# Kernel optimization log

Measured on AMD Instinct MI355X. Metric: run time of the kernel, lower is better.

Reference implementation:

```python
import jax, jax.numpy as jnp
import numpy as np

NEG_SLOPE = 0.2

def gat_layer(x, src, dst, W, a_src, a_dst, b):
    # PyG GATConv (concat=True, self-loops already appended to src/dst)
    N = x.shape[0]
    H, C = a_src.shape
    h = (x @ W).reshape(N, H, C)                      # [N,H,C]
    alpha_s = jnp.einsum('nhc,hc->nh', h, a_src)      # [N,H]
    alpha_d = jnp.einsum('nhc,hc->nh', h, a_dst)
    e = jax.nn.leaky_relu(alpha_s[src] + alpha_d[dst], NEG_SLOPE)  # [E,H]
    # scatter-softmax over edges grouped by destination node
    m = jax.ops.segment_max(e, dst, num_segments=N)
    e = jnp.exp(e - m[dst])
    denom = jax.ops.segment_sum(e, dst, num_segments=N)
    alpha = e / (denom[dst] + 1e-16)                  # [E,H]
    msg = h[src] * alpha[:, :, None]                  # [E,H,C]
    out = jax.ops.segment_sum(msg, dst, num_segments=N)
    return out.reshape(N, H * C) + b


def setup_inputs() -> dict:
    key = jax.random.key(0)
    ks = jax.random.split(key, 16)
    N, E, B = 20000, 640000, 32
    in_f, out_dim = 128, 512
    x = jax.random.normal(ks[0], (N, in_f), dtype=jnp.float32)
    edge_index = jax.random.randint(ks[1], (2, E), 0, N, dtype=jnp.int64)
    batch = jnp.sort(jax.random.randint(ks[2], (N,), 0, B, dtype=jnp.int64))
    def p(k, shape):
        return jax.random.normal(k, shape, dtype=jnp.float32) * 0.1
    inp = {
        'x': x, 'edge_index': edge_index, 'batch': batch,
        'W1': p(ks[3], (in_f, 256)), 'a1_src': p(ks[4], (4, 64)), 'a1_dst': p(ks[5], (4, 64)), 'b1': jnp.zeros((256,), jnp.float32),
        'W2': p(ks[6], (256, 256)), 'a2_src': p(ks[7], (4, 64)), 'a2_dst': p(ks[8], (4, 64)), 'b2': jnp.zeros((256,), jnp.float32),
        'W3': p(ks[9], (256, 256)), 'a3_src': p(ks[10], (4, 64)), 'a3_dst': p(ks[11], (4, 64)), 'b3': jnp.zeros((256,), jnp.float32),
        'W4': p(ks[12], (256, 512)), 'a4_src': p(ks[13], (4, 128)), 'a4_dst': p(ks[14], (4, 128)), 'b4': jnp.zeros((512,), jnp.float32),
        'fcW': p(ks[15], (1024, out_dim)), 'fcb': jnp.zeros((out_dim,), jnp.float32),
    }
    return inp


def reference(x, edge_index, batch, W1, a1_src, a1_dst, b1, W2, a2_src, a2_dst, b2,
              W3, a3_src, a3_dst, b3, W4, a4_src, a4_dst, b4, fcW, fcb):
    N = x.shape[0]
    B = 32
    loops = jnp.arange(N, dtype=edge_index.dtype)
    src = jnp.concatenate([edge_index[0], loops])
    dst = jnp.concatenate([edge_index[1], loops])
    h = jax.nn.elu(gat_layer(x, src, dst, W1, a1_src, a1_dst, b1))
    h = jax.nn.elu(gat_layer(h, src, dst, W2, a2_src, a2_dst, b2))
    h = jax.nn.elu(gat_layer(h, src, dst, W3, a3_src, a3_dst, b3))
    h = jax.nn.elu(gat_layer(h, src, dst, W4, a4_src, a4_dst, b4))   # [N,512]
    cnt = jax.ops.segment_sum(jnp.ones((N,), h.dtype), batch, num_segments=B)
    x_mean = jax.ops.segment_sum(h, batch, num_segments=B) / jnp.maximum(cnt, 1.0)[:, None]
    x_max = jax.ops.segment_max(h, batch, num_segments=B)
    x_max = jnp.where(jnp.isfinite(x_max), x_max, 0.0)
    g = jnp.concatenate([x_mean, x_max], axis=1)                     # [B,1024]
    return g @ fcW + fcb
```

## Files before the change

kernel.cpp:

```cpp
#include <hip/hip_runtime.h>
#include <math.h>

#define WAVE 64

typedef __attribute__((ext_vector_type(4))) float f32x4;
typedef _Float16 h16x4 __attribute__((ext_vector_type(4)));
typedef _Float16 h16x8 __attribute__((ext_vector_type(8)));

__device__ __forceinline__ float selh(float e0, float e1, float e2, float e3, int m){
  float r = (m == 1) ? e1 : e0;
  r = (m == 2) ? e2 : r;
  r = (m == 3) ? e3 : r;
  return r;
}

__global__ void k_zero_i(int* p, int n){
  int i = blockIdx.x*blockDim.x + threadIdx.x;
  if (i < n) p[i] = 0;
}

__global__ void k_zero_f(float* p, int n){
  int i = blockIdx.x*blockDim.x + threadIdx.x;
  if (i < n) p[i] = 0.f;
}

__global__ void k_count(const int* __restrict__ ei, int E, int N, int* __restrict__ cnt){
  int i = blockIdx.x*blockDim.x + threadIdx.x;
  if (i >= E + N) return;
  int d = (i < E) ? ei[E + i] : (i - E);
  atomicAdd(&cnt[d], 1);
}

__global__ __launch_bounds__(1024)
void k_scan1(const int* __restrict__ cnt, int* __restrict__ rp, int* __restrict__ bsum, int N){
  __shared__ int sd[1024];
  int t = threadIdx.x, i = blockIdx.x*1024 + t;
  int v = (i < N) ? cnt[i] : 0;
  sd[t] = v;
  __syncthreads();
  for (int off = 1; off < 1024; off <<= 1){
    int x = (t >= off) ? sd[t-off] : 0;
    __syncthreads();
    sd[t] += x;
    __syncthreads();
  }
  if (i < N) rp[i] = sd[t] - v;
  if (t == 1023) bsum[blockIdx.x] = sd[1023];
}

__global__ void k_scan2(int* __restrict__ bsum, int nb, int* __restrict__ rp, int N){
  int t = threadIdx.x;
  int orig = (t < nb) ? bsum[t] : 0;
  int v = orig;
  #pragma unroll
  for (int off = 1; off < 64; off <<= 1){
    int x = __shfl_up(v, off, WAVE);
    if (t >= off) v += x;
  }
  if (t < nb) bsum[t] = v - orig;
  if (t == 63) rp[N] = v;
}

__global__ __launch_bounds__(1024)
void k_scan3(int* __restrict__ rp, const int* __restrict__ bsum, int N){
  int i = blockIdx.x*1024 + threadIdx.x;
  if (i < N) rp[i] += bsum[blockIdx.x];
}

__global__ void k_copy_i(const int* __restrict__ a, int* __restrict__ b, int n){
  int i = blockIdx.x*blockDim.x + threadIdx.x;
  if (i < n) b[i] = a[i];
}

__global__ void k_fill(const int* __restrict__ ei, int E, int N,
                       int* __restrict__ cur, int* __restrict__ es){
  int i = blockIdx.x*blockDim.x + threadIdx.x;
  if (i >= E + N) return;
  int s, d;
  if (i < E){ s = ei[i]; d = ei[E + i]; } else { s = d = i - E; }
  int pos = atomicAdd(&cur[d], 1);
  es[pos] = s;
}

__global__ void k_bounds(const int* __restrict__ batch, int N, int B, int* __restrict__ bs){
  int b = blockIdx.x*blockDim.x + threadIdx.x;
  if (b > B) return;
  int lo = 0, hi = N;
  while (lo < hi){ int mid = (lo + hi) >> 1; if (batch[mid] < b) lo = mid + 1; else hi = mid; }
  bs[b] = lo;
}

__global__ __launch_bounds__(256)
void k_cvt16(const float* __restrict__ in, _Float16* __restrict__ out, int n4){
  int i = blockIdx.x*blockDim.x + threadIdx.x;
  if (i >= n4) return;
  float4 v = ((const float4*)in)[i];
  h16x4 o;
  o[0] = (_Float16)v.x; o[1] = (_Float16)v.y;
  o[2] = (_Float16)v.z; o[3] = (_Float16)v.w;
  ((h16x4*)out)[i] = o;
}

__global__ __launch_bounds__(256)
void k_cvt_w16(const float* __restrict__ W, _Float16* __restrict__ wt, int K, int Nc){
  int i = blockIdx.x*blockDim.x + threadIdx.x;
  if (i >= K*Nc) return;
  int k = i / Nc, n = i - k*Nc;
  wt[(size_t)n*K + k] = (_Float16)W[i];
}

template<int CHEAD>
__global__ __launch_bounds__(512)
void k_gemm_fused(const _Float16* __restrict__ Ax, const _Float16* __restrict__ Bw,
                  _Float16* __restrict__ Ch,
                  const float* __restrict__ asr, const float* __restrict__ adt,
                  float* __restrict__ as4, float* __restrict__ ad4,
                  int M, int K, int Nc){
  constexpr int LDP = 40;
  __shared__ _Float16 sA[128*LDP], sB[128*LDP];
  const int tid = threadIdx.x;
  const int m0 = blockIdx.x*128, n0 = blockIdx.y*128;
  const int w = tid >> 6, l = tid & 63;
  const int wr = w >> 1, wc = w & 1;
  const int sr = tid >> 2, sc = (tid & 3)*8;

  f32x4 acc00={0.f,0.f,0.f,0.f}, acc01=acc00, acc02=acc00, acc03=acc00;
  f32x4 acc10=acc00, acc11=acc00, acc12=acc00, acc13=acc00;

  const int arow = m0 + sr;
  const bool aval = arow < M;
  const size_t aoff = (size_t)arow*K + sc;
  const size_t boff = (size_t)(n0 + sr)*K + sc;

  const int fa0 = (wr*32 + (l & 15))*LDP + (l >> 4)*8;
  const int fa1 = fa0 + 16*LDP;
  const int fb0 = (wc*64 + (l & 15))*LDP + (l >> 4)*8;

  for (int k0 = 0; k0 < K; k0 += 32){
    uint4 va = make_uint4(0,0,0,0);
    if (aval) va = *(const uint4*)(Ax + aoff + k0);
    uint4 vb = *(const uint4*)(Bw + boff + k0);
    __syncthreads();
    *(uint4*)&sA[sr*LDP + sc] = va;
    *(uint4*)&sB[sr*LDP + sc] = vb;
    __syncthreads();

    h16x8 a0 = *(const h16x8*)&sA[fa0];
    h16x8 a1 = *(const h16x8*)&sA[fa1];

    h16x8 b;
    b = *(const h16x8*)&sB[fb0];
    acc00 = __builtin_amdgcn_mfma_f32_16x16x32_f16(a0, b, acc00, 0, 0, 0);
    acc10 = __builtin_amdgcn_mfma_f32_16x16x32_f16(a1, b, acc10, 0, 0, 0);
    b = *(const h16x8*)&sB[fb0 + 16*LDP];
    acc01 = __builtin_amdgcn_mfma_f32_16x16x32_f16(a0, b, acc01, 0, 0, 0);
    acc11 = __builtin_amdgcn_mfma_f32_16x16x32_f16(a1, b, acc11, 0, 0, 0);
    b = *(const h16x8*)&sB[fb0 + 32*LDP];
    acc02 = __builtin_amdgcn_mfma_f32_16x16x32_f16(a0, b, acc02, 0, 0, 0);
    acc12 = __builtin_amdgcn_mfma_f32_16x16x32_f16(a1, b, acc12, 0, 0, 0);
    b = *(const h16x8*)&sB[fb0 + 48*LDP];
    acc03 = __builtin_amdgcn_mfma_f32_16x16x32_f16(a0, b, acc03, 0, 0, 0);
    acc13 = __builtin_amdgcn_mfma_f32_16x16x32_f16(a1, b, acc13, 0, 0, 0);
  }

  const int colb = n0 + wc*64 + (l & 15);
  const int hy = (n0 + wc*64) / CHEAD;
  const float ca0 = asr[colb], ca1 = asr[colb+16], ca2 = asr[colb+32], ca3 = asr[colb+48];
  const float cd0 = adt[colb], cd1 = adt[colb+16], cd2 = adt[colb+32], cd3 = adt[colb+48];

  {
    const int rb = m0 + wr*32 + (l >> 4)*4;
    #pragma unroll
    for (int j = 0; j < 4; ++j){
      int row = rb + j;
      if (row < M){
        _Float16* hp = Ch + (size_t)row*Nc + colb;
        hp[0]  = (_Float16)acc00[j];
        hp[16] = (_Float16)acc01[j];
        hp[32] = (_Float16)acc02[j];
        hp[48] = (_Float16)acc03[j];
      }
      float ps = ca0*acc00[j] + ca1*acc01[j] + ca2*acc02[j] + ca3*acc03[j];
      float pd = cd0*acc00[j] + cd1*acc01[j] + cd2*acc02[j] + cd3*acc03[j];
      ps += __shfl_xor(ps, 1, WAVE);  pd += __shfl_xor(pd, 1, WAVE);
      ps += __shfl_xor(ps, 2, WAVE);  pd += __shfl_xor(pd, 2, WAVE);
      ps += __shfl_xor(ps, 4, WAVE);  pd += __shfl_xor(pd, 4, WAVE);
      ps += __shfl_xor(ps, 8, WAVE);  pd += __shfl_xor(pd, 8, WAVE);
      if ((l & 15) == 0 && row < M){
        atomicAdd(&as4[(size_t)row*4 + hy], ps);
        atomicAdd(&ad4[(size_t)row*4 + hy], pd);
      }
    }
  }
  {
    const int rb = m0 + wr*32 + 16 + (l >> 4)*4;
    #pragma unroll
    for (int j = 0; j < 4; ++j){
      int row = rb + j;
      if (row < M){
        _Float16* hp = Ch + (size_t)row*Nc + colb;
        hp[0]  = (_Float16)acc10[j];
        hp[16] = (_Float16)acc11[j];
        hp[32] = (_Float16)acc12[j];
        hp[48] = (_Float16)acc13[j];
      }
      float ps = ca0*acc10[j] + ca1*acc11[j] + ca2*acc12[j] + ca3*acc13[j];
      float pd = cd0*acc10[j] + cd1*acc11[j] + cd2*acc12[j] + cd3*acc13[j];
      ps += __shfl_xor(ps, 1, WAVE);  pd += __shfl_xor(pd, 1, WAVE);
      ps += __shfl_xor(ps, 2, WAVE);  pd += __shfl_xor(pd, 2, WAVE);
      ps += __shfl_xor(ps, 4, WAVE);  pd += __shfl_xor(pd, 4, WAVE);
      ps += __shfl_xor(ps, 8, WAVE);  pd += __shfl_xor(pd, 8, WAVE);
      if ((l & 15) == 0 && row < M){
        atomicAdd(&as4[(size_t)row*4 + hy], ps);
        atomicAdd(&ad4[(size_t)row*4 + hy], pd);
      }
    }
  }
}

template<int HC, int WF32>
__global__ __launch_bounds__(256)
void k_agg_h(const int* __restrict__ rp, const int* __restrict__ es,
             const float* __restrict__ as4, const float* __restrict__ ad4,
             const _Float16* __restrict__ h, const float* __restrict__ bias,
             float* __restrict__ outF, _Float16* __restrict__ oH, int N){
  constexpr int VEC = HC / 64;
  int wid  = (blockIdx.x*blockDim.x + threadIdx.x) >> 6;
  int lane = threadIdx.x & 63;
  if (wid >= N) return;
  int beg = rp[wid], end = rp[wid+1];

  const float4 adv = *(const float4*)(ad4 + (size_t)wid*4);
  const float ad0 = adv.x, ad1 = adv.y, ad2 = adv.z, ad3 = adv.w;

  float m0=-1e30f, m1=-1e30f, m2=-1e30f, m3=-1e30f;
  float s0=0.f, s1=0.f, s2=0.f, s3=0.f;
  for (int i = beg + lane; i < end; i += WAVE){
    int s = es[i];
    const float4 av = *(const float4*)(as4 + (size_t)s*4);
    float e, mn;
    e = av.x + ad0; e = (e >= 0.f) ? e : 0.2f*e;
    mn = fmaxf(m0, e); s0 = s0*__expf(m0-mn) + __expf(e-mn); m0 = mn;
    e = av.y + ad1; e = (e >= 0.f) ? e : 0.2f*e;
    mn = fmaxf(m1, e); s1 = s1*__expf(m1-mn) + __expf(e-mn); m1 = mn;
    e = av.z + ad2; e = (e >= 0.f) ? e : 0.2f*e;
    mn = fmaxf(m2, e); s2 = s2*__expf(m2-mn) + __expf(e-mn); m2 = mn;
    e = av.w + ad3; e = (e >= 0.f) ? e : 0.2f*e;
    mn = fmaxf(m3, e); s3 = s3*__expf(m3-mn) + __expf(e-mn); m3 = mn;
  }
  #pragma unroll
  for (int off = 32; off > 0; off >>= 1){
    float mo, so, mn;
    mo = __shfl_xor(m0, off, WAVE); so = __shfl_xor(s0, off, WAVE);
    mn = fmaxf(m0, mo); s0 = s0*__expf(m0-mn) + so*__expf(mo-mn); m0 = mn;
    mo = __shfl_xor(m1, off, WAVE); so = __shfl_xor(s1, off, WAVE);
    mn = fmaxf(m1, mo); s1 = s1*__expf(m1-mn) + so*__expf(mo-mn); m1 = mn;
    mo = __shfl_xor(m2, off, WAVE); so = __shfl_xor(s2, off, WAVE);
    mn = fmaxf(m2, mo); s2 = s2*__expf(m2-mn) + so*__expf(mo-mn); m2 = mn;
    mo = __shfl_xor(m3, off, WAVE); so = __shfl_xor(s3, off, WAVE);
    mn = fmaxf(m3, mo); s3 = s3*__expf(m3-mn) + so*__expf(mo-mn); m3 = mn;
  }
  const float i0 = 1.f/(s0 + 1e-16f), i1 = 1.f/(s1 + 1e-16f);
  const float i2 = 1.f/(s2 + 1e-16f), i3 = 1.f/(s3 + 1e-16f);
  const int myh = lane >> 4;

  float ac[VEC] = {};

  for (int cb = beg; cb < end; cb += WAVE){
    int nn = min(WAVE, end - cb);
    int sidx = 0;
    float w0 = 0.f, w1 = 0.f, w2 = 0.f, w3 = 0.f;
    if (cb + lane < end){
      sidx = es[cb + lane];
      const float4 av = *(const float4*)(as4 + (size_t)sidx*4);
      float e;
      e = av.x + ad0; e = (e >= 0.f) ? e : 0.2f*e; w0 = __expf(e - m0)*i0;
      e = av.y + ad1; e = (e >= 0.f) ? e : 0.2f*e; w1 = __expf(e - m1)*i1;
      e = av.z + ad2; e = (e >= 0.f) ? e : 0.2f*e; w2 = __expf(e - m2)*i2;
      e = av.w + ad3; e = (e >= 0.f) ? e : 0.2f*e; w3 = __expf(e - m3)*i3;
    }

    int j = 0;
    for (; j + 4 <= nn; j += 4){
      int sj0 = __shfl(sidx, j+0, WAVE), sj1 = __shfl(sidx, j+1, WAVE);
      int sj2 = __shfl(sidx, j+2, WAVE), sj3 = __shfl(sidx, j+3, WAVE);
      float u0 = selh(__shfl(w0,j+0,WAVE), __shfl(w1,j+0,WAVE), __shfl(w2,j+0,WAVE), __shfl(w3,j+0,WAVE), myh);
      float u1 = selh(__shfl(w0,j+1,WAVE), __shfl(w1,j+1,WAVE), __shfl(w2,j+1,WAVE), __shfl(w3,j+1,WAVE), myh);
      float u2 = selh(__shfl(w0,j+2,WAVE), __shfl(w1,j+2,WAVE), __shfl(w2,j+2,WAVE), __shfl(w3,j+2,WAVE), myh);
      float u3 = selh(__shfl(w0,j+3,WAVE), __shfl(w1,j+3,WAVE), __shfl(w2,j+3,WAVE), __shfl(w3,j+3,WAVE), myh);
      if (VEC == 4){
        h16x4 v0 = *(const h16x4*)(h + (size_t)sj0*HC + lane*4);
        h16x4 v1 = *(const h16x4*)(h + (size_t)sj1*HC + lane*4);
        h16x4 v2 = *(const h16x4*)(h + (size_t)sj2*HC + lane*4);
        h16x4 v3 = *(const h16x4*)(h + (size_t)sj3*HC + lane*4);
        #pragma unroll
        for (int c = 0; c < 4; ++c)
          ac[c] = fmaf(u0,(float)v0[c], fmaf(u1,(float)v1[c], fmaf(u2,(float)v2[c], fmaf(u3,(float)v3[c], ac[c]))));
      } else {
        h16x8 v0 = *(const h16x8*)(h + (size_t)sj0*HC + lane*8);
        h16x8 v1 = *(const h16x8*)(h + (size_t)sj1*HC + lane*8);
        h16x8 v2 = *(const h16x8*)(h + (size_t)sj2*HC + lane*8);
        h16x8 v3 = *(const h16x8*)(h + (size_t)sj3*HC + lane*8);
        #pragma unroll
        for (int c = 0; c < VEC; ++c)
          ac[c] = fmaf(u0,(float)v0[c], fmaf(u1,(float)v1[c], fmaf(u2,(float)v2[c], fmaf(u3,(float)v3[c], ac[c]))));
      }
    }
    for (; j < nn; ++j){
      int sj = __shfl(sidx, j, WAVE);
      float u = selh(__shfl(w0,j,WAVE), __shfl(w1,j,WAVE), __shfl(w2,j,WAVE), __shfl(w3,j,WAVE), myh);
      if (VEC == 4){
        h16x4 v = *(const h16x4*)(h + (size_t)sj*HC + lane*4);
        #pragma unroll
        for (int c = 0; c < 4; ++c) ac[c] = fmaf(u, (float)v[c], ac[c]);
      } else {
        h16x8 v = *(const h16x8*)(h + (size_t)sj*HC + lane*8);
        #pragma unroll
        for (int c = 0; c < VEC; ++c) ac[c] = fmaf(u, (float)v[c], ac[c]);
      }
    }
  }

  float r0=0,r1=0,r2=0,r3=0,r4=0,r5=0,r6=0,r7=0;
  {
    const float* bp = bias + lane*VEC;
    #pragma unroll
    for (int c = 0; c < VEC; ++c){
      float r = ac[c] + bp[c];
      r = r > 0.f ? r : expm1f(r);
      if (c==0) r0=r; else if (c==1) r1=r; else if (c==2) r2=r; else if (c==3) r3=r;
      else if (c==4) r4=r; else if (c==5) r5=r; else if (c==6) r6=r; else r7=r;
    }
  }
  if (WF32){
    float* op = outF + (size_t)wid*HC + lane*VEC;
    *(float4*)op = make_float4(r0,r1,r2,r3);
    if (VEC == 8) *(float4*)(op+4) = make_float4(r4,r5,r6,r7);
  } else {
    h16x4 o;
    o[0] = (_Float16)r0; o[1] = (_Float16)r1;
    o[2] = (_Float16)r2; o[3] = (_Float16)r3;
    *(h16x4*)(oH + (size_t)wid*HC + lane*VEC) = o;
    if (VEC == 8){
      h16x4 o2;
      o2[0] = (_Float16)r4; o2[1] = (_Float16)r5;
      o2[2] = (_Float16)r6; o2[3] = (_Float16)r7;
      *(h16x4*)(oH + (size_t)wid*HC + lane*VEC + 4) = o2;
    }
  }
}

__global__ void k_pool_partial(const float* __restrict__ h, const int* __restrict__ bs,
                               float* __restrict__ psum, float* __restrict__ pmax){
  int b = blockIdx.x, ch = blockIdx.y;
  int f = threadIdx.x;
  int s = bs[b], e = bs[b+1];
  long long len = e - s;
  int i0 = s + (int)(len * ch / 8);
  int i1 = s + (int)(len * (ch+1) / 8);
  float sm = 0.f, mx = -3.0e38f;
  for (int i = i0; i < i1; ++i){
    float v = h[(size_t)i*512 + f];
    sm += v; mx = fmaxf(mx, v);
  }
  int idx = (b*8 + ch)*512 + f;
  psum[idx] = sm; pmax[idx] = mx;
}

__global__ void k_pool_final(const float* __restrict__ psum, const float* __restrict__ pmax,
                             const int* __restrict__ bs, float* __restrict__ g){
  int b = blockIdx.x, f = threadIdx.x;
  float sm = 0.f, mx = -3.0e38f;
  for (int c = 0; c < 8; ++c){
    int idx = (b*8 + c)*512 + f;
    sm += psum[idx]; mx = fmaxf(mx, pmax[idx]);
  }
  int cnt = bs[b+1] - bs[b];
  g[b*1024 + f] = sm / fmaxf((float)cnt, 1.f);
  g[b*1024 + 512 + f] = (mx > -1e37f) ? mx : 0.f;
}

__global__ __launch_bounds__(256)
void k_fc(const float* __restrict__ g, const float* __restrict__ fcW,
          const float* __restrict__ fcb, float* __restrict__ out){
  __shared__ float gs[1024];
  __shared__ float red[4][64];
  int b = blockIdx.x, t = threadIdx.x;
  int o0 = blockIdx.y * 64;
  for (int i = t; i < 1024; i += 256) gs[i] = g[b*1024 + i];
  __syncthreads();
  int ol = t & 63, q = t >> 6;
  const float* wp = fcW + (size_t)(q*256)*512 + o0 + ol;
  float acc = 0.f;
  #pragma unroll 8
  for (int k = 0; k < 256; ++k)
    acc = fmaf(gs[q*256 + k], wp[(size_t)k*512], acc);
  red[q][ol] = acc;
  __syncthreads();
  if (t < 64){
    float r = red[0][t] + red[1][t] + red[2][t] + red[3][t] + fcb[o0 + t];
    out[b*512 + o0 + t] = r;
  }
}

extern "C" void kernel_launch(void* const* d_in, const int* in_sizes, int n_in,
                              void* d_out, int out_size, void* d_ws, size_t ws_size,
                              hipStream_t stream){
  (void)n_in; (void)out_size; (void)ws_size;
  const float* x     = (const float*)d_in[0];
  const int*   ei    = (const int*)d_in[1];
  const int*   batch = (const int*)d_in[2];
  const float* W[4]   = {(const float*)d_in[3],(const float*)d_in[7],(const float*)d_in[11],(const float*)d_in[15]};
  const float* asr[4] = {(const float*)d_in[4],(const float*)d_in[8],(const float*)d_in[12],(const float*)d_in[16]};
  const float* adt[4] = {(const float*)d_in[5],(const float*)d_in[9],(const float*)d_in[13],(const float*)d_in[17]};
  const float* bb[4]  = {(const float*)d_in[6],(const float*)d_in[10],(const float*)d_in[14],(const float*)d_in[18]};
  const float* fcW = (const float*)d_in[19];
  const float* fcb = (const float*)d_in[20];

  const int N  = in_sizes[0] / 128;
  const int E  = in_sizes[1] / 2;
  const int EN = E + N;
  const int B  = 32;
  const int NB = (N + 1023) / 1024;

  char* p = (char*)d_ws;
  auto alloc = [&](size_t bytes){ void* r = (void*)p; p += (bytes + 255) & ~(size_t)255; return r; };
  float* bufA = (float*)alloc((size_t)N*512*4);
  _Float16* hA = (_Float16*)alloc((size_t)N*512*2);
  _Float16* hB = (_Float16*)alloc((size_t)N*512*2);
  _Float16* Wh = (_Float16*)alloc((size_t)512*256*2);
  float* a2   = (float*)alloc((size_t)N*8*4);
  float* as4 = a2;
  float* ad4 = a2 + (size_t)N*4;
  int*   cnt  = (int*)alloc((size_t)N*4);
  int*   rp   = (int*)alloc((size_t)(N+1)*4);
  int*   cur  = (int*)alloc((size_t)N*4);
  int*   es   = (int*)alloc((size_t)EN*4);
  int*   bs   = (int*)alloc((size_t)(B+1)*4);
  int*   bsum = (int*)alloc((size_t)64*4);
  float* gpo  = (float*)alloc((size_t)B*1024*4);
  float* psum = (float*)alloc((size_t)B*8*512*4);
  float* pmax = (float*)alloc((size_t)B*8*512*4);

  k_zero_i<<<(N+255)/256, 256, 0, stream>>>(cnt, N);
  k_count<<<(EN+255)/256, 256, 0, stream>>>(ei, E, N, cnt);
  k_scan1<<<NB, 1024, 0, stream>>>(cnt, rp, bsum, N);
  k_scan2<<<1, 64, 0, stream>>>(bsum, NB, rp, N);
  k_scan3<<<NB, 1024, 0, stream>>>(rp, bsum, N);
  k_copy_i<<<(N+255)/256, 256, 0, stream>>>(rp, cur, N);
  k_fill<<<(EN+255)/256, 256, 0, stream>>>(ei, E, N, cur, es);
  k_bounds<<<1, 64, 0, stream>>>(batch, N, B, bs);

  const int wgrid = (N + 3) / 4;

  k_cvt16<<<((N*128/4) + 255)/256, 256, 0, stream>>>(x, hB, N*128/4);

  const int Kd[4]  = {128, 256, 256, 256};
  const int HCd[4] = {256, 256, 256, 512};

  for (int L = 0; L < 4; ++L){
    const int K = Kd[L], Nc = HCd[L];
    k_zero_f<<<(N*8 + 255)/256, 256, 0, stream>>>(a2, N*8);
    k_cvt_w16<<<(K*Nc + 255)/256, 256, 0, stream>>>(W[L], Wh, K, Nc);
    dim3 gg((N + 127)/128, Nc/128);
    if (Nc == 256)
      k_gemm_fused<64><<<gg, 512, 0, stream>>>(hB, Wh, hA, asr[L], adt[L], as4, ad4, N, K, Nc);
    else
      k_gemm_fused<128><<<gg, 512, 0, stream>>>(hB, Wh, hA, asr[L], adt[L], as4, ad4, N, K, Nc);
    if (L < 3)
      k_agg_h<256,0><<<wgrid, 256, 0, stream>>>(rp, es, as4, ad4, hA, bb[L], (float*)nullptr, hB, N);
    else
      k_agg_h<512,1><<<wgrid, 256, 0, stream>>>(rp, es, as4, ad4, hA, bb[L], bufA, (_Float16*)nullptr, N);
  }

  dim3 pg(B, 8);
  k_pool_partial<<<pg, 512, 0, stream>>>(bufA, bs, psum, pmax);
  k_pool_final<<<B, 512, 0, stream>>>(psum, pmax, bs, gpo);
  dim3 fg(B, 8);
  k_fc<<<fg, 256, 0, stream>>>(gpo, fcW, fcb, (float*)d_out);
}
```

Baseline: 490.8 us.

## Double-buffer GEMM LDS, drop attention-logit atomics, batch weight conversion and fuse copies

The GEMM main loop now double-buffers the shared-memory tiles, prefetching the next K slice while MFMAs run, so only one barrier is needed per step. Per-row attention logits are written directly, or reduced through shared memory for the 128-wide heads, instead of accumulated with atomics. This removes the per-layer zeroing kernel. All four weight matrices are converted in a single launch, and the cur copy is folded into the scan fixup kernel, cutting the launch count. The cost is twice the LDS use per block and an extra barrier in the epilogue for the wide-head layer.

After: 447.8 us. 8.8% less time.

```diff
diff --git a/kernel.cpp b/kernel.cpp
--- a/kernel.cpp
+++ b/kernel.cpp
@@ -17,11 +17,6 @@
 __global__ void k_zero_i(int* p, int n){
   int i = blockIdx.x*blockDim.x + threadIdx.x;
   if (i < n) p[i] = 0;
-}
-
-__global__ void k_zero_f(float* p, int n){
-  int i = blockIdx.x*blockDim.x + threadIdx.x;
-  if (i < n) p[i] = 0.f;
 }
 
 __global__ void k_count(const int* __restrict__ ei, int E, int N, int* __restrict__ cnt){
@@ -62,14 +57,13 @@
 }
 
 __global__ __launch_bounds__(1024)
-void k_scan3(int* __restrict__ rp, const int* __restrict__ bsum, int N){
+void k_scan3(int* __restrict__ rp, int* __restrict__ cur, const int* __restrict__ bsum, int N){
   int i = blockIdx.x*1024 + threadIdx.x;
-  if (i < N) rp[i] += bsum[blockIdx.x];
-}
-
-__global__ void k_copy_i(const int* __restrict__ a, int* __restrict__ b, int n){
-  int i = blockIdx.x*blockDim.x + threadIdx.x;
-  if (i < n) b[i] = a[i];
+  if (i < N){
+    int v = rp[i] + bsum[blockIdx.x];
+    rp[i] = v;
+    cur[i] = v;
+  }
 }
 
 __global__ void k_fill(const int* __restrict__ ei, int E, int N,
@@ -102,11 +96,26 @@
 }
 
 __global__ __launch_bounds__(256)
-void k_cvt_w16(const float* __restrict__ W, _Float16* __restrict__ wt, int K, int Nc){
+void k_cvt_w_all(const float* __restrict__ W0, const float* __restrict__ W1,
+                 const float* __restrict__ W2, const float* __restrict__ W3,
+                 _Float16* __restrict__ out){
   int i = blockIdx.x*blockDim.x + threadIdx.x;
-  if (i >= K*Nc) return;
-  int k = i / Nc, n = i - k*Nc;
-  wt[(size_t)n*K + k] = (_Float16)W[i];
+  if (i < 32768){
+    int k = i >> 8, n = i & 255;
+    out[(size_t)n*128 + k] = (_Float16)W0[i];
+  } else if (i < 98304){
+    int j = i - 32768;
+    int k = j >> 8, n = j & 255;
+    out[32768 + (size_t)n*256 + k] = (_Float16)W1[j];
+  } else if (i < 163840){
+    int j = i - 98304;
+    int k = j >> 8, n = j & 255;
+    out[98304 + (size_t)n*256 + k] = (_Float16)W2[j];
+  } else if (i < 294912){
+    int j = i - 163840;
+    int k = j >> 9, n = j & 511;
+    out[163840 + (size_t)n*256 + k] = (_Float16)W3[j];
+  }
 }
 
 template<int CHEAD>
@@ -117,7 +126,7 @@
                   float* __restrict__ as4, float* __restrict__ ad4,
                   int M, int K, int Nc){
   constexpr int LDP = 40;
-  __shared__ _Float16 sA[128*LDP], sB[128*LDP];
+  __shared__ _Float16 sA[2][128*LDP], sB[2][128*LDP];
   const int tid = threadIdx.x;
   const int m0 = blockIdx.x*128, n0 = blockIdx.y*128;
   const int w = tid >> 6, l = tid & 63;
@@ -135,39 +144,55 @@
   const int fa0 = (wr*32 + (l & 15))*LDP + (l >> 4)*8;
   const int fa1 = fa0 + 16*LDP;
   const int fb0 = (wc*64 + (l & 15))*LDP + (l >> 4)*8;
-
-  for (int k0 = 0; k0 < K; k0 += 32){
-    uint4 va = make_uint4(0,0,0,0);
-    if (aval) va = *(const uint4*)(Ax + aoff + k0);
-    uint4 vb = *(const uint4*)(Bw + boff + k0);
-    __syncthreads();
-    *(uint4*)&sA[sr*LDP + sc] = va;
-    *(uint4*)&sB[sr*LDP + sc] = vb;
-    __syncthreads();
-
-    h16x8 a0 = *(const h16x8*)&sA[fa0];
-    h16x8 a1 = *(const h16x8*)&sA[fa1];
-
+  const int steps = K >> 5;
+
+  uint4 va = make_uint4(0,0,0,0), vb;
+  if (aval) va = *(const uint4*)(Ax + aoff);
+  vb = *(const uint4*)(Bw + boff);
+  *(uint4*)&sA[0][sr*LDP + sc] = va;
+  *(uint4*)&sB[0][sr*LDP + sc] = vb;
+  __syncthreads();
+
+  for (int ks = 0; ks < steps; ++ks){
+    const int cur = ks & 1;
+    const bool more = (ks + 1 < steps);
+    if (more){
+      const int k0 = (ks + 1)*32;
+      va = make_uint4(0,0,0,0);
+      if (aval) va = *(const uint4*)(Ax + aoff + k0);
+      vb = *(const uint4*)(Bw + boff + k0);
+    }
+
+    h16x8 a0 = *(const h16x8*)&sA[cur][fa0];
+    h16x8 a1 = *(const h16x8*)&sA[cur][fa1];
     h16x8 b;
-    b = *(const h16x8*)&sB[fb0];
+    b = *(const h16x8*)&sB[cur][fb0];
     acc00 = __builtin_amdgcn_mfma_f32_16x16x32_f16(a0, b, acc00, 0, 0, 0);
     acc10 = __builtin_amdgcn_mfma_f32_16x16x32_f16(a1, b, acc10, 0, 0, 0);
-    b = *(const h16x8*)&sB[fb0 + 16*LDP];
+    b = *(const h16x8*)&sB[cur][fb0 + 16*LDP];
     acc01 = __builtin_amdgcn_mfma_f32_16x16x32_f16(a0, b, acc01, 0, 0, 0);
     acc11 = __builtin_amdgcn_mfma_f32_16x16x32_f16(a1, b, acc11, 0, 0, 0);
-    b = *(const h16x8*)&sB[fb0 + 32*LDP];
+    b = *(const h16x8*)&sB[cur][fb0 + 32*LDP];
     acc02 = __builtin_amdgcn_mfma_f32_16x16x32_f16(a0, b, acc02, 0, 0, 0);
     acc12 = __builtin_amdgcn_mfma_f32_16x16x32_f16(a1, b, acc12, 0, 0, 0);
-    b = *(const h16x8*)&sB[fb0 + 48*LDP];
+    b = *(const h16x8*)&sB[cur][fb0 + 48*LDP];
     acc03 = __builtin_amdgcn_mfma_f32_16x16x32_f16(a0, b, acc03, 0, 0, 0);
     acc13 = __builtin_amdgcn_mfma_f32_16x16x32_f16(a1, b, acc13, 0, 0, 0);
+
+    if (more){
+      *(uint4*)&sA[cur^1][sr*LDP + sc] = va;
+      *(uint4*)&sB[cur^1][sr*LDP + sc] = vb;
+      __syncthreads();
+    }
   }
 
   const int colb = n0 + wc*64 + (l & 15);
-  const int hy = (n0 + wc*64) / CHEAD;
   const float ca0 = asr[colb], ca1 = asr[colb+16], ca2 = asr[colb+32], ca3 = asr[colb+48];
   const float cd0 = adt[colb], cd1 = adt[colb+16], cd2 = adt[colb+32], cd3 = adt[colb+48];
 
+  float psA[1]; (void)psA;
+
+  float psm0[4], pdm0[4], psm1[4], pdm1[4];
   {
     const int rb = m0 + wr*32 + (l >> 4)*4;
     #pragma unroll
@@ -186,10 +211,7 @@
       ps += __shfl_xor(ps, 2, WAVE);  pd += __shfl_xor(pd, 2, WAVE);
       ps += __shfl_xor(ps, 4, WAVE);  pd += __shfl_xor(pd, 4, WAVE);
       ps += __shfl_xor(ps, 8, WAVE);  pd += __shfl_xor(pd, 8, WAVE);
-      if ((l & 15) == 0 && row < M){
-        atomicAdd(&as4[(size_t)row*4 + hy], ps);
-        atomicAdd(&ad4[(size_t)row*4 + hy], pd);
-      }
+      psm0[j] = ps; pdm0[j] = pd;
     }
   }
   {
@@ -210,9 +232,51 @@
       ps += __shfl_xor(ps, 2, WAVE);  pd += __shfl_xor(pd, 2, WAVE);
       ps += __shfl_xor(ps, 4, WAVE);  pd += __shfl_xor(pd, 4, WAVE);
       ps += __shfl_xor(ps, 8, WAVE);  pd += __shfl_xor(pd, 8, WAVE);
-      if ((l & 15) == 0 && row < M){
-        atomicAdd(&as4[(size_t)row*4 + hy], ps);
-        atomicAdd(&ad4[(size_t)row*4 + hy], pd);
+      psm1[j] = ps; pdm1[j] = pd;
+    }
+  }
+
+  if (CHEAD == 64){
+    const int hy = blockIdx.y*2 + wc;
+    if ((l & 15) == 0){
+      const int rb0 = m0 + wr*32 + (l >> 4)*4;
+      #pragma unroll
+      for (int j = 0; j < 4; ++j){
+        int row = rb0 + j;
+        if (row < M){ as4[(size_t)row*4 + hy] = psm0[j]; ad4[(size_t)row*4 + hy] = pdm0[j]; }
+      }
+      const int rb1 = rb0 + 16;
+      #pragma unroll
+      for (int j = 0; j < 4; ++j){
+        int row = rb1 + j;
+        if (row < M){ as4[(size_t)row*4 + hy] = psm1[j]; ad4[(size_t)row*4 + hy] = pdm1[j]; }
+      }
+    }
+  } else {
+    float* red = (float*)&sA[0][0];
+    __syncthreads();
+    if ((l & 15) == 0){
+      const int lr0 = wr*32 + (l >> 4)*4;
+      #pragma unroll
+      for (int j = 0; j < 4; ++j){
+        red[(lr0 + j)*4 + wc*2 + 0] = psm0[j];
+        red[(lr0 + j)*4 + wc*2 + 1] = pdm0[j];
+      }
+      const int lr1 = lr0 + 16;
+      #pragma unroll
+      for (int j = 0; j < 4; ++j){
+        red[(lr1 + j)*4 + wc*2 + 0] = psm1[j];
+        red[(lr1 + j)*4 + wc*2 + 1] = pdm1[j];
+      }
+    }
+    __syncthreads();
+    if (tid < 128){
+      int row = m0 + tid;
+      if (row < M){
+        float ps = red[tid*4 + 0] + red[tid*4 + 2];
+        float pd = red[tid*4 + 1] + red[tid*4 + 3];
+        as4[(size_t)row*4 + blockIdx.y] = ps;
+        ad4[(size_t)row*4 + blockIdx.y] = pd;
       }
     }
   }
@@ -428,7 +492,7 @@
   float* bufA = (float*)alloc((size_t)N*512*4);
   _Float16* hA = (_Float16*)alloc((size_t)N*512*2);
   _Float16* hB = (_Float16*)alloc((size_t)N*512*2);
-  _Float16* Wh = (_Float16*)alloc((size_t)512*256*2);
+  _Float16* Wh = (_Float16*)alloc((size_t)294912*2);
   float* a2   = (float*)alloc((size_t)N*8*4);
   float* as4 = a2;
   float* ad4 = a2 + (size_t)N*4;
@@ -446,27 +510,25 @@
   k_count<<<(EN+255)/256, 256, 0, stream>>>(ei, E, N, cnt);
   k_scan1<<<NB, 1024, 0, stream>>>(cnt, rp, bsum, N);
   k_scan2<<<1, 64, 0, stream>>>(bsum, NB, rp, N);
-  k_scan3<<<NB, 1024, 0, stream>>>(rp, bsum, N);
-  k_copy_i<<<(N+255)/256, 256, 0, stream>>>(rp, cur, N);
+  k_scan3<<<NB, 1024, 0, stream>>>(rp, cur, bsum, N);
   k_fill<<<(EN+255)/256, 256, 0, stream>>>(ei, E, N, cur, es);
   k_bounds<<<1, 64, 0, stream>>>(batch, N, B, bs);
 
+  k_cvt16<<<((N*128/4) + 255)/256, 256, 0, stream>>>(x, hB, N*128/4);
+  k_cvt_w_all<<<(294912 + 255)/256, 256, 0, stream>>>(W[0], W[1], W[2], W[3], Wh);
+
   const int wgrid = (N + 3) / 4;
-
-  k_cvt16<<<((N*128/4) + 255)/256, 256, 0, stream>>>(x, hB, N*128/4);
-
   const int Kd[4]  = {128, 256, 256, 256};
   const int HCd[4] = {256, 256, 256, 512};
+  const size_t Woff[4] = {0, 32768, 98304, 163840};
 
   for (int L = 0; L < 4; ++L){
     const int K = Kd[L], Nc = HCd[L];
-    k_zero_f<<<(N*8 + 255)/256, 256, 0, stream>>>(a2, N*8);
-    k_cvt_w16<<<(K*Nc + 255)/256, 256, 0, stream>>>(W[L], Wh, K, Nc);
     dim3 gg((N + 127)/128, Nc/128);
     if (Nc == 256)
-      k_gemm_fused<64><<<gg, 512, 0, stream>>>(hB, Wh, hA, asr[L], adt[L], as4, ad4, N, K, Nc);
+      k_gemm_fused<64><<<gg, 512, 0, stream>>>(hB, Wh + Woff[L], hA, asr[L], adt[L], as4, ad4, N, K, Nc);
     else
-      k_gemm_fused<128><<<gg, 512, 0, stream>>>(hB, Wh, hA, asr[L], adt[L], as4, ad4, N, K, Nc);
+      k_gemm_fused<128><<<gg, 512, 0, stream>>>(hB, Wh + Woff[L], hA, asr[L], adt[L], as4, ad4, N, K, Nc);
     if (L < 3)
       k_agg_h<256,0><<<wgrid, 256, 0, stream>>>(rp, es, as4, ad4, hA, bb[L], (float*)nullptr, hB, N);
     else
```
